# Optimization experiments

Hardware: AMD Instinct MI355X
Metric: run time of the kernel (lower is better)

Reference implementation:

```python
import jax, jax.numpy as jnp
import numpy as np

B, C, D = 16384, 2048, 256
THR = 0.8       # threshold
M_NEG = 0.3     # margin_neg (margin_pos is unused in the original forward)
EPS = 1e-8      # torch.nn.CosineSimilarity norm clamp


def setup_inputs() -> dict:
    key = jax.random.key(0)
    k1, k2 = jax.random.split(key)
    preds = jax.random.normal(k1, (B, D), dtype=jnp.float32)
    cls = jax.random.randint(k2, (B,), 0, C)
    labels = jax.nn.one_hot(cls, C, dtype=jnp.float32)  # [B, C] one-hot soft labels
    return {"preds": preds, "labels": labels}


def reference(preds, labels):
    # --- append(): running-mean centroids over rows with labels >= THR ---
    # The sequential EMA with counter c -> c/(c+1)*old + 1/(c+1)*new is exactly the
    # arithmetic mean of the contributing preds, so compute it as a masked mean.
    mask = labels >= THR                                  # [B, C]
    cnt = mask.sum(axis=0)                                # [C]
    exists = cnt > 0                                      # which centroids exist in the dict
    maskf = mask.astype(preds.dtype)
    centroids = (maskf.T @ preds) / jnp.maximum(cnt, 1).astype(preds.dtype)[:, None]  # [C, D]

    pn = preds / jnp.maximum(jnp.linalg.norm(preds, axis=1, keepdims=True), EPS)  # [B, D]

    # --- dist_positive: 1 - cos(pred, sum_{label>0} label[c] * centroid[c]) ---
    cmb = jnp.where(labels > 0, labels, 0.0) @ centroids  # [B, D]
    cmbn = cmb / jnp.maximum(jnp.linalg.norm(cmb, axis=1, keepdims=True), EPS)
    pos = 1.0 - jnp.sum(pn * cmbn, axis=1)                # [B]

    # --- dist_negative: mean over existing centroids with label < 1-THR of
    #     relu(margin_neg - (1 - cos(pred, centroid))) ---
    cn = centroids / jnp.maximum(jnp.linalg.norm(centroids, axis=1, keepdims=True), EPS)
    cos_all = pn @ cn.T                                   # [B, C]
    neg_mask = (labels < 1.0 - THR) & exists[None, :]     # [B, C]
    hinge = jnp.maximum(M_NEG - (1.0 - cos_all), 0.0)
    adds = jnp.maximum(neg_mask.sum(axis=1), 1).astype(preds.dtype)  # [B]
    neg = (hinge * neg_mask).sum(axis=1) / adds           # [B]

    return jnp.mean(pos) + jnp.mean(neg)
```

## Files before the change

### kernel.cpp

```cpp
#include <hip/hip_runtime.h>
#include <hip/hip_bf16.h>

constexpr int BB = 16384;
constexpr int CC = 2048;
constexpr int DD = 256;
constexpr float THR   = 0.8f;
constexpr float EPSN  = 1e-8f;

typedef __bf16 bf16x8 __attribute__((ext_vector_type(8)));
typedef float  f32x4  __attribute__((ext_vector_type(4)));

constexpr int ROWSLOTS = 64;

__global__ __launch_bounds__(256) void k_findcls(const float* __restrict__ labels,
                                                 int* __restrict__ cls,
                                                 int* __restrict__ cnt,
                                                 int* __restrict__ rowlist) {
  constexpr size_t total = (size_t)BB * CC / 4;
  size_t q = (size_t)blockIdx.x * blockDim.x + threadIdx.x;
  size_t stride = (size_t)gridDim.x * blockDim.x;
  const float4* l4 = reinterpret_cast<const float4*>(labels);
  for (; q < total; q += stride) {
    float4 v = l4[q];
    if (v.x >= THR || v.y >= THR || v.z >= THR || v.w >= THR) {
      int f = (int)(q * 4);
      int row = f >> 11;
      int col = f & (CC - 1);
      int c = col + (v.x >= THR ? 0 : v.y >= THR ? 1 : v.z >= THR ? 2 : 3);
      cls[row] = c;
      int s = atomicAdd(&cnt[c], 1);
      if (s < ROWSLOTS) rowlist[c * ROWSLOTS + s] = row;
    }
  }
}

__global__ __launch_bounds__(256) void k_pn(const float* __restrict__ preds,
                                            unsigned short* __restrict__ pn) {
  int b = blockIdx.x * 4 + (threadIdx.x >> 6);
  int lane = threadIdx.x & 63;
  float4 v = reinterpret_cast<const float4*>(preds + (size_t)b * DD)[lane];
  float s = v.x * v.x + v.y * v.y + v.z * v.z + v.w * v.w;
#pragma unroll
  for (int o = 32; o > 0; o >>= 1) s += __shfl_xor(s, o);
  float inv = 1.0f / fmaxf(sqrtf(s), EPSN);
  union { ushort4 u4; unsigned short us[4]; } o;
  float f0 = v.x * inv, f1 = v.y * inv, f2 = v.z * inv, f3 = v.w * inv;
  __bf16 h0 = (__bf16)f0, h1 = (__bf16)f1, h2 = (__bf16)f2, h3 = (__bf16)f3;
  o.us[0] = *reinterpret_cast<unsigned short*>(&h0);
  o.us[1] = *reinterpret_cast<unsigned short*>(&h1);
  o.us[2] = *reinterpret_cast<unsigned short*>(&h2);
  o.us[3] = *reinterpret_cast<unsigned short*>(&h3);
  reinterpret_cast<ushort4*>(pn + (size_t)b * DD)[lane] = o.u4;
}

__global__ __launch_bounds__(256) void k_cn(
    const float* __restrict__ preds, const int* __restrict__ cnt,
    const int* __restrict__ rowlist, unsigned short* __restrict__ cn,
    int* __restrict__ exists, int* __restrict__ Ecnt) {
  int c = blockIdx.x;
  int t = threadIdx.x;
  int n = cnt[c];
  int nn = n < ROWSLOTS ? n : ROWSLOTS;
  float sum = 0.f;
  for (int i = 0; i < nn; ++i) {
    int row = rowlist[c * ROWSLOTS + i];
    sum += preds[(size_t)row * DD + t];
  }
  float mean = sum / (float)(n > 0 ? n : 1);
  float s = mean * mean;
#pragma unroll
  for (int o = 32; o > 0; o >>= 1) s += __shfl_xor(s, o);
  __shared__ float red[4];
  int wave = t >> 6, lane = t & 63;
  if (lane == 0) red[wave] = s;
  __syncthreads();
  float tot = red[0] + red[1] + red[2] + red[3];
  float inv = 1.0f / fmaxf(sqrtf(tot), EPSN);
  __bf16 h = (__bf16)(mean * inv);
  cn[c * DD + t] = *reinterpret_cast<unsigned short*>(&h);
  if (t == 0) {
    exists[c] = (n > 0) ? 1 : 0;
    if (n > 0) atomicAdd(Ecnt, 1);
  }
}


__device__ __forceinline__ void stage16(char* lds, const char* gsrc_row0, int tid) {
#pragma unroll
  for (int i = 0; i < 4; ++i) {
    int L = i * 4096 + tid * 16;
    int row = L >> 7;
    int cb  = (L & 127) ^ ((row & 7) << 4);
    const char* g = gsrc_row0 + (size_t)row * (DD * 2) + cb;
    __builtin_amdgcn_global_load_lds(
        (const __attribute__((address_space(1))) unsigned int*)g,
        (__attribute__((address_space(3))) unsigned int*)(lds + L), 16, 0, 0);
  }
}

__device__ __forceinline__ bf16x8 ldfrag(const char* buf, int row, int cb) {
  return *reinterpret_cast<const bf16x8*>(buf + row * 128 + (cb ^ ((row & 7) << 4)));
}

__global__ __launch_bounds__(256) void k_loss(
    const unsigned short* __restrict__ pn, const unsigned short* __restrict__ cn,
    const int* __restrict__ cls, const int* __restrict__ exists,
    const int* __restrict__ Ecnt, float* __restrict__ out) {
  constexpr int BM = 128, BN = 128;
  __shared__ __align__(16) char sA[BM * 64 * 2];
  __shared__ __align__(16) char sB[BN * 64 * 2];

  int bid = blockIdx.x;
  int nb = (bid & 7) * (2048 / 8) + (bid >> 3);
  int mtile = nb % (BB / BM);
  int ntile = nb / (BB / BM);
  int rowbase = mtile * BM, colbase = ntile * BN;
  int tid = threadIdx.x, w = tid >> 6, lane = tid & 63;
  int r16 = lane & 15, khi = lane >> 4;
  int wr0 = w * 32 + r16;

  const char* pnB = (const char*)pn + (size_t)rowbase * (DD * 2);
  const char* cnB = (const char*)cn + (size_t)colbase * (DD * 2);

  f32x4 acc[2][8];
#pragma unroll
  for (int i = 0; i < 2; ++i)
#pragma unroll
    for (int j = 0; j < 8; ++j) acc[i][j] = {0.f, 0.f, 0.f, 0.f};

#pragma unroll
  for (int ks = 0; ks < 4; ++ks) {
    stage16(sA, pnB + ks * 128, tid);
    stage16(sB, cnB + ks * 128, tid);
    __syncthreads();
#pragma unroll
    for (int kk = 0; kk < 2; ++kk) {
      int cb = khi * 16 + kk * 64;
      bf16x8 a0 = ldfrag(sA, wr0, cb);
      bf16x8 a1 = ldfrag(sA, wr0 + 16, cb);
#pragma unroll
      for (int j = 0; j < 8; ++j) {
        bf16x8 bj = ldfrag(sB, j * 16 + r16, cb);
        acc[0][j] = __builtin_amdgcn_mfma_f32_16x16x32_bf16(a0, bj, acc[0][j], 0, 0, 0);
        acc[1][j] = __builtin_amdgcn_mfma_f32_16x16x32_bf16(a1, bj, acc[1][j], 0, 0, 0);
      }
    }
    if (ks < 3) __syncthreads();
  }

  int E = *Ecnt;
  float inv_B = 1.0f / (float)BB;
  float inv_neg = inv_B / (float)((E - 1) > 0 ? (E - 1) : 1);
  int grow0 = rowbase + w * 32;

  int clsr[2][4];
#pragma unroll
  for (int i = 0; i < 2; ++i)
#pragma unroll
    for (int r = 0; r < 4; ++r) clsr[i][r] = cls[grow0 + i * 16 + khi * 4 + r];
  int exs[8];
#pragma unroll
  for (int j = 0; j < 8; ++j) exs[j] = exists[colbase + j * 16 + r16];

  float local = 0.f;
#pragma unroll
  for (int i = 0; i < 2; ++i)
#pragma unroll
    for (int j = 0; j < 8; ++j) {
      int ccol = colbase + j * 16 + r16;
#pragma unroll
      for (int r = 0; r < 4; ++r) {
        float v = acc[i][j][r];
        if (ccol == clsr[i][r])
          local += (1.0f - v) * inv_B;
        else if (exs[j])
          local += fmaxf(v - 0.7f, 0.f) * inv_neg;
      }
    }

#pragma unroll
  for (int o = 32; o > 0; o >>= 1) local += __shfl_xor(local, o);
  __shared__ float red[4];
  if (lane == 0) red[w] = local;
  __syncthreads();
  if (tid == 0) atomicAdd(out, red[0] + red[1] + red[2] + red[3]);
}

extern "C" void kernel_launch(void* const* d_in, const int* in_sizes, int n_in,
                              void* d_out, int out_size, void* d_ws, size_t ws_size,
                              hipStream_t stream) {
  const float* preds  = (const float*)d_in[0];
  const float* labels = (const float*)d_in[1];
  float* out = (float*)d_out;

  char* ws = (char*)d_ws;
  int*            cnt     = (int*)(ws + 0);
  int*            Ecnt    = (int*)(ws + 8192);
  int*            cls     = (int*)(ws + 8256);
  int*            rowlist = (int*)(ws + 73792);
  int*            exists  = (int*)(ws + 598080);
  unsigned short* pn      = (unsigned short*)(ws + 606272);
  unsigned short* cn      = (unsigned short*)(ws + 8994880);

  hipMemsetAsync(ws, 0, 8256, stream);
  hipMemsetAsync(d_out, 0, sizeof(float), stream);

  k_findcls<<<2048, 256, 0, stream>>>(labels, cls, cnt, rowlist);
  k_pn<<<BB / 4, 256, 0, stream>>>(preds, pn);
  k_cn<<<CC, 256, 0, stream>>>(preds, cnt, rowlist, cn, exists, Ecnt);
  k_loss<<<(BB / 128) * (CC / 128), 256, 0, stream>>>(pn, cn, cls, exists, Ecnt, out);
}
```

Measured before the change: 109.3 us.

## Enlarge GEMM tiles with double-buffered LDS and merge prep kernels

The loss GEMM moves from 128x128 tiles with 256 threads to 256x256 tiles with 512 threads. Each wave now computes an 8x4 fragment grid, and LDS is double-buffered so the next K-slice loads while MFMAs run. The label scan and pred normalisation kernels are merged into one launch that also zeroes the output, which drops a memset and a launch. The larger tiles give only 512 blocks and raise register pressure, so occupancy and wave balance may suffer.

```diff
diff --git a/kernel.cpp b/kernel.cpp
--- a/kernel.cpp
+++ b/kernel.cpp
@@ -12,45 +12,47 @@
 
 constexpr int ROWSLOTS = 64;
 
-__global__ __launch_bounds__(256) void k_findcls(const float* __restrict__ labels,
-                                                 int* __restrict__ cls,
-                                                 int* __restrict__ cnt,
-                                                 int* __restrict__ rowlist) {
-  constexpr size_t total = (size_t)BB * CC / 4;
-  size_t q = (size_t)blockIdx.x * blockDim.x + threadIdx.x;
-  size_t stride = (size_t)gridDim.x * blockDim.x;
-  const float4* l4 = reinterpret_cast<const float4*>(labels);
-  for (; q < total; q += stride) {
-    float4 v = l4[q];
-    if (v.x >= THR || v.y >= THR || v.z >= THR || v.w >= THR) {
-      int f = (int)(q * 4);
-      int row = f >> 11;
-      int col = f & (CC - 1);
-      int c = col + (v.x >= THR ? 0 : v.y >= THR ? 1 : v.z >= THR ? 2 : 3);
-      cls[row] = c;
-      int s = atomicAdd(&cnt[c], 1);
-      if (s < ROWSLOTS) rowlist[c * ROWSLOTS + s] = row;
-    }
-  }
-}
-
-__global__ __launch_bounds__(256) void k_pn(const float* __restrict__ preds,
-                                            unsigned short* __restrict__ pn) {
-  int b = blockIdx.x * 4 + (threadIdx.x >> 6);
-  int lane = threadIdx.x & 63;
-  float4 v = reinterpret_cast<const float4*>(preds + (size_t)b * DD)[lane];
-  float s = v.x * v.x + v.y * v.y + v.z * v.z + v.w * v.w;
-#pragma unroll
-  for (int o = 32; o > 0; o >>= 1) s += __shfl_xor(s, o);
-  float inv = 1.0f / fmaxf(sqrtf(s), EPSN);
-  union { ushort4 u4; unsigned short us[4]; } o;
-  float f0 = v.x * inv, f1 = v.y * inv, f2 = v.z * inv, f3 = v.w * inv;
-  __bf16 h0 = (__bf16)f0, h1 = (__bf16)f1, h2 = (__bf16)f2, h3 = (__bf16)f3;
-  o.us[0] = *reinterpret_cast<unsigned short*>(&h0);
-  o.us[1] = *reinterpret_cast<unsigned short*>(&h1);
-  o.us[2] = *reinterpret_cast<unsigned short*>(&h2);
-  o.us[3] = *reinterpret_cast<unsigned short*>(&h3);
-  reinterpret_cast<ushort4*>(pn + (size_t)b * DD)[lane] = o.u4;
+__global__ __launch_bounds__(256) void k_prep(const float* __restrict__ labels,
+                                              const float* __restrict__ preds,
+                                              int* __restrict__ cls,
+                                              int* __restrict__ cnt,
+                                              int* __restrict__ rowlist,
+                                              unsigned short* __restrict__ pn,
+                                              float* __restrict__ out) {
+  if (blockIdx.x < 2048) {
+    if (blockIdx.x == 0 && threadIdx.x == 0) *out = 0.f;
+    constexpr size_t total = (size_t)BB * CC / 4;
+    size_t q = (size_t)blockIdx.x * 256 + threadIdx.x;
+    const float4* l4 = reinterpret_cast<const float4*>(labels);
+    for (; q < total; q += 2048 * 256) {
+      float4 v = l4[q];
+      if (v.x >= THR || v.y >= THR || v.z >= THR || v.w >= THR) {
+        int f = (int)(q * 4);
+        int row = f >> 11;
+        int col = f & (CC - 1);
+        int c = col + (v.x >= THR ? 0 : v.y >= THR ? 1 : v.z >= THR ? 2 : 3);
+        cls[row] = c;
+        int s = atomicAdd(&cnt[c], 1);
+        if (s < ROWSLOTS) rowlist[c * ROWSLOTS + s] = row;
+      }
+    }
+  } else {
+    int b = (blockIdx.x - 2048) * 4 + (threadIdx.x >> 6);
+    int lane = threadIdx.x & 63;
+    float4 v = reinterpret_cast<const float4*>(preds + (size_t)b * DD)[lane];
+    float s = v.x * v.x + v.y * v.y + v.z * v.z + v.w * v.w;
+#pragma unroll
+    for (int o = 32; o > 0; o >>= 1) s += __shfl_xor(s, o);
+    float inv = 1.0f / fmaxf(sqrtf(s), EPSN);
+    union { ushort4 u4; unsigned short us[4]; } o;
+    float f0 = v.x * inv, f1 = v.y * inv, f2 = v.z * inv, f3 = v.w * inv;
+    __bf16 h0 = (__bf16)f0, h1 = (__bf16)f1, h2 = (__bf16)f2, h3 = (__bf16)f3;
+    o.us[0] = *reinterpret_cast<unsigned short*>(&h0);
+    o.us[1] = *reinterpret_cast<unsigned short*>(&h1);
+    o.us[2] = *reinterpret_cast<unsigned short*>(&h2);
+    o.us[3] = *reinterpret_cast<unsigned short*>(&h3);
+    reinterpret_cast<ushort4*>(pn + (size_t)b * DD)[lane] = o.u4;
+  }
 }
 
 __global__ __launch_bounds__(256) void k_cn(
@@ -85,105 +87,124 @@
 }
 
 
-__device__ __forceinline__ void stage16(char* lds, const char* gsrc_row0, int tid) {
+__device__ __forceinline__ void stage32k(char* lds, const char* gsrc_row0,
+                                         int tid, int ksbyte) {
 #pragma unroll
   for (int i = 0; i < 4; ++i) {
-    int L = i * 4096 + tid * 16;
+    int L = i * 8192 + tid * 16;
     int row = L >> 7;
-    int cb  = (L & 127) ^ ((row & 7) << 4);
-    const char* g = gsrc_row0 + (size_t)row * (DD * 2) + cb;
+    int kb  = (L & 127) ^ ((row & 7) << 4);
+    const char* g = gsrc_row0 + (size_t)row * (DD * 2) + ksbyte + kb;
     __builtin_amdgcn_global_load_lds(
         (const __attribute__((address_space(1))) unsigned int*)g,
         (__attribute__((address_space(3))) unsigned int*)(lds + L), 16, 0, 0);
   }
 }
 
-__device__ __forceinline__ bf16x8 ldfrag(const char* buf, int row, int cb) {
-  return *reinterpret_cast<const bf16x8*>(buf + row * 128 + (cb ^ ((row & 7) << 4)));
-}
-
-__global__ __launch_bounds__(256) void k_loss(
+__device__ __forceinline__ bf16x8 ldfrag(const char* buf, int row, int kb) {
+  return *reinterpret_cast<const bf16x8*>(buf + row * 128 + (kb ^ ((row & 7) << 4)));
+}
+
+__global__ __launch_bounds__(512, 2) void k_loss(
     const unsigned short* __restrict__ pn, const unsigned short* __restrict__ cn,
     const int* __restrict__ cls, const int* __restrict__ exists,
     const int* __restrict__ Ecnt, float* __restrict__ out) {
-  constexpr int BM = 128, BN = 128;
-  __shared__ __align__(16) char sA[BM * 64 * 2];
-  __shared__ __align__(16) char sB[BN * 64 * 2];
+  constexpr int BM = 256, BN = 256;
+  __shared__ __align__(16) char sA[2][BM * 64 * 2];
+  __shared__ __align__(16) char sB[2][BN * 64 * 2];
+  __shared__ float red[8];
 
   int bid = blockIdx.x;
-  int nb = (bid & 7) * (2048 / 8) + (bid >> 3);
-  int mtile = nb % (BB / BM);
-  int ntile = nb / (BB / BM);
+  int nb = (bid & 7) * 64 + (bid >> 3);
+  int mtile = nb & 63;
+  int ntile = nb >> 6;
   int rowbase = mtile * BM, colbase = ntile * BN;
   int tid = threadIdx.x, w = tid >> 6, lane = tid & 63;
+  int wm = w >> 2, wn = w & 3;
   int r16 = lane & 15, khi = lane >> 4;
-  int wr0 = w * 32 + r16;
+  int arow0 = wm * 128 + r16;
+  int brow0 = wn * 64 + r16;
 
   const char* pnB = (const char*)pn + (size_t)rowbase * (DD * 2);
   const char* cnB = (const char*)cn + (size_t)colbase * (DD * 2);
 
-  f32x4 acc[2][8];
-#pragma unroll
-  for (int i = 0; i < 2; ++i)
-#pragma unroll
-    for (int j = 0; j < 8; ++j) acc[i][j] = {0.f, 0.f, 0.f, 0.f};
-
+  f32x4 acc[8][4];
+#pragma unroll
+  for (int m = 0; m < 8; ++m)
+#pragma unroll
+    for (int n = 0; n < 4; ++n) acc[m][n] = {0.f, 0.f, 0.f, 0.f};
+
+  stage32k(sA[0], pnB, tid, 0);
+  stage32k(sB[0], cnB, tid, 0);
+  __syncthreads();
+
+  int cur = 0;
 #pragma unroll
   for (int ks = 0; ks < 4; ++ks) {
-    stage16(sA, pnB + ks * 128, tid);
-    stage16(sB, cnB + ks * 128, tid);
+    if (ks < 3) {
+      stage32k(sA[cur ^ 1], pnB, tid, (ks + 1) * 128);
+      stage32k(sB[cur ^ 1], cnB, tid, (ks + 1) * 128);
+    }
+    const char* bufA = sA[cur];
+    const char* bufB = sB[cur];
+#pragma unroll
+    for (int kk = 0; kk < 2; ++kk) {
+      int kb = kk * 64 + khi * 16;
+      bf16x8 b[4];
+#pragma unroll
+      for (int n = 0; n < 4; ++n) b[n] = ldfrag(bufB, brow0 + n * 16, kb);
+#pragma unroll
+      for (int m = 0; m < 8; ++m) {
+        bf16x8 a = ldfrag(bufA, arow0 + m * 16, kb);
+#pragma unroll
+        for (int n = 0; n < 4; ++n)
+          acc[m][n] = __builtin_amdgcn_mfma_f32_16x16x32_bf16(a, b[n], acc[m][n], 0, 0, 0);
+      }
+    }
     __syncthreads();
-#pragma unroll
-    for (int kk = 0; kk < 2; ++kk) {
-      int cb = khi * 16 + kk * 64;
-      bf16x8 a0 = ldfrag(sA, wr0, cb);
-      bf16x8 a1 = ldfrag(sA, wr0 + 16, cb);
-#pragma unroll
-      for (int j = 0; j < 8; ++j) {
-        bf16x8 bj = ldfrag(sB, j * 16 + r16, cb);
-        acc[0][j] = __builtin_amdgcn_mfma_f32_16x16x32_bf16(a0, bj, acc[0][j], 0, 0, 0);
-        acc[1][j] = __builtin_amdgcn_mfma_f32_16x16x32_bf16(a1, bj, acc[1][j], 0, 0, 0);
-      }
-    }
-    if (ks < 3) __syncthreads();
+    cur ^= 1;
   }
 
   int E = *Ecnt;
   float inv_B = 1.0f / (float)BB;
   float inv_neg = inv_B / (float)((E - 1) > 0 ? (E - 1) : 1);
-  int grow0 = rowbase + w * 32;
-
-  int clsr[2][4];
-#pragma unroll
-  for (int i = 0; i < 2; ++i)
-#pragma unroll
-    for (int r = 0; r < 4; ++r) clsr[i][r] = cls[grow0 + i * 16 + khi * 4 + r];
-  int exs[8];
-#pragma unroll
-  for (int j = 0; j < 8; ++j) exs[j] = exists[colbase + j * 16 + r16];
+  int grow0 = rowbase + wm * 128;
+
+  int clsr[8][4];
+#pragma unroll
+  for (int m = 0; m < 8; ++m)
+#pragma unroll
+    for (int r = 0; r < 4; ++r) clsr[m][r] = cls[grow0 + m * 16 + khi * 4 + r];
+  int exs[4];
+#pragma unroll
+  for (int n = 0; n < 4; ++n) exs[n] = exists[colbase + wn * 64 + n * 16 + r16];
 
   float local = 0.f;
 #pragma unroll
-  for (int i = 0; i < 2; ++i)
-#pragma unroll
-    for (int j = 0; j < 8; ++j) {
-      int ccol = colbase + j * 16 + r16;
+  for (int m = 0; m < 8; ++m)
+#pragma unroll
+    for (int n = 0; n < 4; ++n) {
+      int ccol = colbase + wn * 64 + n * 16 + r16;
 #pragma unroll
       for (int r = 0; r < 4; ++r) {
-        float v = acc[i][j][r];
-        if (ccol == clsr[i][r])
+        float v = acc[m][n][r];
+        if (ccol == clsr[m][r])
           local += (1.0f - v) * inv_B;
-        else if (exs[j])
+        else if (exs[n])
           local += fmaxf(v - 0.7f, 0.f) * inv_neg;
       }
     }
 
 #pragma unroll
   for (int o = 32; o > 0; o >>= 1) local += __shfl_xor(local, o);
-  __shared__ float red[4];
   if (lane == 0) red[w] = local;
   __syncthreads();
-  if (tid == 0) atomicAdd(out, red[0] + red[1] + red[2] + red[3]);
+  if (tid == 0) {
+    float t = 0.f;
+#pragma unroll
+    for (int i = 0; i < 8; ++i) t += red[i];
+    atomicAdd(out, t);
+  }
 }
 
 extern "C" void kernel_launch(void* const* d_in, const int* in_sizes, int n_in,
@@ -203,10 +224,7 @@
   unsigned short* cn      = (unsigned short*)(ws + 8994880);
 
   hipMemsetAsync(ws, 0, 8256, stream);
-  hipMemsetAsync(d_out, 0, sizeof(float), stream);
-
-  k_findcls<<<2048, 256, 0, stream>>>(labels, cls, cnt, rowlist);
-  k_pn<<<BB / 4, 256, 0, stream>>>(preds, pn);
+  k_prep<<<6144, 256, 0, stream>>>(labels, preds, cls, cnt, rowlist, pn, out);
   k_cn<<<CC, 256, 0, stream>>>(preds, cnt, rowlist, cn, exists, Ecnt);
-  k_loss<<<(BB / 128) * (CC / 128), 256, 0, stream>>>(pn, cn, cls, exists, Ecnt, out);
-}
+  k_loss<<<512, 512, 0, stream>>>(pn, cn, cls, exists, Ecnt, out);
+}
```

Measured after the change: 96.25 us (median of 2 runs). -11.9%, faster.
